# Kernel tuning notes

Hardware: AMD Instinct MI355X
Metric: run time of the kernel (lower is better)

The kernel has to match this reference:

```python
import jax, jax.numpy as jnp
import numpy as np

BS, NUM_VISIT, MAX_FEAT, MAX_TARGET = 32, 6, 12, 16
NUM_FEAT, NUM_REL, HIDDEN, REDUCED, OUT = 1992, 11, 128, 256, 90
GAMMA = 0.1


def setup_inputs() -> dict:
    key = jax.random.key(0)
    ks = jax.random.split(key, 20)
    u = lambda k, shape: jax.random.uniform(k, shape, dtype=jnp.float32)
    # one/multi-hot-like dense float inputs (per docstring)
    feat_index = (u(ks[0], (BS, NUM_VISIT, MAX_FEAT, NUM_FEAT)) < 0.01).astype(jnp.float32)
    neighbor_index = (u(ks[1], (BS, NUM_VISIT, MAX_FEAT, MAX_TARGET, NUM_FEAT)) < 0.001).astype(jnp.float32)
    rel_index = (u(ks[2], (BS, NUM_VISIT, MAX_FEAT, MAX_TARGET, NUM_REL)) < 0.2).astype(jnp.float32)
    # parameters (torch.rand init in the original; xavier for embedding)
    bound = float(np.sqrt(6.0 / (NUM_FEAT + HIDDEN)))
    emb_weight = jax.random.uniform(ks[3], (NUM_FEAT, HIDDEN), dtype=jnp.float32, minval=-bound, maxval=bound)
    return {
        "feat_index": feat_index,
        "neighbor_index": neighbor_index,
        "rel_index": rel_index,
        "emb_weight": emb_weight,
        "W_edge": u(ks[4], (NUM_REL, HIDDEN)),
        "W_v": u(ks[5], (REDUCED, HIDDEN)),
        "W_r": u(ks[6], (REDUCED, HIDDEN)),
        "b_v": u(ks[7], (REDUCED,)),
        "b_r": u(ks[8], (REDUCED,)),
        "W_alpha": u(ks[9], (NUM_FEAT,)),
        "b_alpha": u(ks[10], (MAX_FEAT,)),
        "W_beta": u(ks[11], (MAX_FEAT,)),
        "b_beta": u(ks[12], (NUM_VISIT,)),
        "W_l": u(ks[13], (REDUCED, REDUCED)),
        "b_l": u(ks[14], (REDUCED,)),
        "fc_W": u(ks[15], (OUT, 2 * REDUCED)) * 0.05,
        "fc_b": u(ks[16], (OUT,)) * 0.05,
    }


def reference(feat_index, neighbor_index, rel_index, emb_weight, W_edge, W_v, W_r,
              b_v, b_r, W_alpha, b_alpha, W_beta, b_beta, W_l, b_l, fc_W, fc_b):
    num_visit = feat_index.shape[1]
    # decay buffer lamb[i] = exp(-gamma*(num_visit - i))
    lamb = jnp.exp(-GAMMA * (num_visit - jnp.arange(num_visit, dtype=feat_index.dtype)))

    # node-level attention alpha: (b,v,m)
    alpha = jax.nn.softmax(jnp.einsum('n,bvmn->bvm', W_alpha, feat_index) + b_alpha)
    # visit-level attention beta: (b,v), modulated by temporal decay
    beta = jnp.tanh(jnp.einsum('m,bvm->bv', W_beta, alpha) + b_beta) * lamb

    # reduced node embeddings: (num_feat, reduced)
    reduced_emb = emb_weight @ W_v.T + b_v
    # attention-weighted neighbor aggregation; sum over targets t fused in
    attn = alpha * beta[:, :, None]                       # (b,v,m)
    node_agg = jnp.einsum('bvm,bvmtn,nr->bvmr', attn, neighbor_index, reduced_emb)

    # reduced edge (relation) embeddings: (num_rel, reduced)
    reduced_edge = W_edge @ W_r.T + b_r
    edge_agg = jnp.einsum('bvmtr,rd->bvmd', rel_index, reduced_edge)  # sum over t fused

    agg = node_agg + edge_agg                             # (b,v,m,reduced)
    # einsum('dd, bvfd -> bvfd') in torch takes the diagonal of W_l
    h = jax.nn.relu(jnp.diagonal(W_l) * agg + b_l)        # (b,v,m,reduced)

    h_g = h.sum(axis=(1, 2))                              # (b, reduced)
    # einsum('bvmn,bvmr->bvnr').sum(n).sum(v) == contract over v,m,n
    h_p = jnp.einsum('bvm,bvmr->br', feat_index.sum(-1), h)

    z_joint = jnp.concatenate([h_g, h_p], axis=-1)        # (b, 2*reduced)
    return jax.nn.sigmoid(z_joint @ fc_W.T + fc_b)
```

## Files before the change

### kernel.cpp

```cpp
#include <hip/hip_runtime.h>
#include <math.h>

#define BS   32
#define NV   6
#define MF   12
#define MT   16
#define NF   1992
#define NR   11
#define HID  128
#define RED  256
#define OUTD 90
#define GAMMA 0.1f
#define NZCAP 512

typedef float f4_t __attribute__((ext_vector_type(4)));

#define WS_HG    0
#define WS_HP    (WS_HG + BS*RED)
#define WS_ATTN  (WS_HP + BS*RED)
#define WS_FSUM  (WS_ATTN + BS*NV*MF)
#define WS_REMB  (WS_FSUM + BS*NV*MF)
#define WS_REDGE (WS_REMB + NF*RED)
#define WS_FCWT  (WS_REDGE + NR*RED)
#define WS_DIAG  (WS_FCWT + 2*RED*OUTD)

#define N_ZERO (2*BS*RED)
#define N_FCWT (2*RED*OUTD)
#define ZERO_BLOCKS (N_ZERO/256)
#define PREP2_BLOCKS ((N_FCWT+RED)/256)
#define ATTN_BLOCKS (BS*NV)
#define NPB 8
#define REMB_BLOCKS (NF/NPB)
#define REDGE_BLOCKS 2
#define K1_BLOCKS (ZERO_BLOCKS+PREP2_BLOCKS+ATTN_BLOCKS+REMB_BLOCKS+REDGE_BLOCKS)

__global__ __launch_bounds__(256) void k1_prep_attn_reduce(
        const float* __restrict__ feat, const float* __restrict__ W_alpha,
        const float* __restrict__ b_alpha, const float* __restrict__ W_beta,
        const float* __restrict__ b_beta,
        const float* __restrict__ emb, const float* __restrict__ W_edge,
        const float* __restrict__ W_v, const float* __restrict__ W_r,
        const float* __restrict__ b_v, const float* __restrict__ b_r,
        const float* __restrict__ fc_W, const float* __restrict__ W_l,
        float* __restrict__ ws_base, float* __restrict__ fcWT,
        float* __restrict__ diag,
        float* __restrict__ attn_ws, float* __restrict__ fsum_ws,
        float* __restrict__ remb, float* __restrict__ redge) {
    int blk = blockIdx.x;
    int tid = threadIdx.x;

    __shared__ float dot12[MF], fs12[MF];
    __shared__ float rows[NPB][HID];
    __shared__ float wT[32][RED + 1];

    if (blk < ZERO_BLOCKS) {
        ws_base[blk * 256 + tid] = 0.f;
        return;
    }
    blk -= ZERO_BLOCKS;

    if (blk < PREP2_BLOCKS) {
        int i = blk * 256 + tid;
        if (i < N_FCWT) {
            int jj = i / OUTD, o = i - jj * OUTD;
            fcWT[i] = fc_W[o * (2 * RED) + jj];
        } else {
            int j = i - N_FCWT;
            diag[j] = W_l[(size_t)j * RED + j];
        }
        return;
    }
    blk -= PREP2_BLOCKS;

    if (blk < ATTN_BLOCKS) {
        int bv   = blk;
        int v    = bv % NV;
        int wave = tid >> 6;
        int lane = tid & 63;
        const float* base = feat + (size_t)bv * MF * NF;
        for (int m = wave; m < MF; m += 4) {
            const float4* rw = (const float4*)(base + (size_t)m * NF);
            const float4* wa = (const float4*)W_alpha;
            float da = 0.f, fs = 0.f;
            for (int i = lane; i < NF / 4; i += 64) {
                float4 x = rw[i];
                float4 w = wa[i];
                da += w.x * x.x + w.y * x.y + w.z * x.z + w.w * x.w;
                fs += x.x + x.y + x.z + x.w;
            }
            #pragma unroll
            for (int off = 32; off > 0; off >>= 1) {
                da += __shfl_xor(da, off);
                fs += __shfl_xor(fs, off);
            }
            if (lane == 0) { dot12[m] = da; fs12[m] = fs; }
        }
        __syncthreads();
        if (tid == 0) {
            float logits[MF];
            float mx = -1e30f;
            for (int m = 0; m < MF; ++m) { logits[m] = dot12[m] + b_alpha[m]; mx = fmaxf(mx, logits[m]); }
            float s = 0.f;
            for (int m = 0; m < MF; ++m) { logits[m] = expf(logits[m] - mx); s += logits[m]; }
            float inv = 1.f / s;
            float bdot = 0.f;
            for (int m = 0; m < MF; ++m) { logits[m] *= inv; bdot += W_beta[m] * logits[m]; }
            float lamb = expf(-GAMMA * (float)(NV - v));
            float beta = tanhf(bdot + b_beta[v]) * lamb;
            for (int m = 0; m < MF; ++m) {
                attn_ws[bv * MF + m] = logits[m] * beta;
                fsum_ws[bv * MF + m] = fs12[m];
            }
        }
        return;
    }
    blk -= ATTN_BLOCKS;

    bool isEdge = (blk >= REMB_BLOCKS);
    const float* src  = isEdge ? W_edge : emb;
    const float* Wm   = isEdge ? W_r : W_v;
    const float* bias = isEdge ? b_r : b_v;
    float* dst        = isEdge ? redge : remb;
    int n0    = (isEdge ? (blk - REMB_BLOCKS) : blk) * NPB;
    int rowsN = isEdge ? min(NPB, NR - n0) : NPB;

    for (int idx = tid; idx < rowsN * HID; idx += 256)
        rows[idx >> 7][idx & 127] = src[(size_t)n0 * HID + idx];

    float bb = bias[tid];
    float a0 = bb, a1 = bb, a2 = bb, a3 = bb, a4 = bb, a5 = bb, a6 = bb, a7 = bb;
    for (int k0 = 0; k0 < HID; k0 += 32) {
        for (int idx = tid; idx < 32 * RED; idx += 256) {
            int rr = idx >> 5, kk = idx & 31;
            wT[kk][rr] = Wm[rr * HID + k0 + kk];
        }
        __syncthreads();
        #pragma unroll
        for (int kk = 0; kk < 32; ++kk) {
            float w = wT[kk][tid];
            int k = k0 + kk;
            a0 += rows[0][k] * w; a1 += rows[1][k] * w;
            a2 += rows[2][k] * w; a3 += rows[3][k] * w;
            a4 += rows[4][k] * w; a5 += rows[5][k] * w;
            a6 += rows[6][k] * w; a7 += rows[7][k] * w;
        }
        __syncthreads();
    }
    float* d0 = dst + (size_t)n0 * RED + tid;
    if (0 < rowsN) d0[0 * RED] = a0;
    if (1 < rowsN) d0[1 * RED] = a1;
    if (2 < rowsN) d0[2 * RED] = a2;
    if (3 < rowsN) d0[3 * RED] = a3;
    if (4 < rowsN) d0[4 * RED] = a4;
    if (5 < rowsN) d0[5 * RED] = a5;
    if (6 < rowsN) d0[6 * RED] = a6;
    if (7 < rowsN) d0[7 * RED] = a7;
}

__global__ __launch_bounds__(256) void k2_stream_gather(
        const float* __restrict__ nbr, const float* __restrict__ rel,
        const float* __restrict__ remb, const float* __restrict__ redge,
        const float* __restrict__ attn_ws, const float* __restrict__ fsum_ws,
        const float* __restrict__ diag, const float* __restrict__ b_l,
        float* __restrict__ h_g, float* __restrict__ h_p) {
    int bvm = blockIdx.x;
    int b   = bvm / (NV * MF);
    int tid = threadIdx.x;
    __shared__ int   nz_n[NZCAP];
    __shared__ float nz_v[NZCAP];
    __shared__ float rsum_s[NR];
    __shared__ int   cnt;
    __shared__ float s_attn, s_fsum;
    if (tid == 0) { cnt = 0; s_attn = attn_ws[bvm]; s_fsum = fsum_ws[bvm]; }

    int r = tid;
    float dg = diag[r];
    float bl = b_l[r];
    float rg[NR];
    #pragma unroll
    for (int j = 0; j < NR; ++j) rg[j] = redge[j * RED + r];

    const f4_t* base = (const f4_t*)(nbr + (size_t)bvm * MT * NF);
    f4_t a0 = (f4_t)(0.f);
    f4_t a1 = (f4_t)(0.f);
    const bool has1 = (tid + 256) < (NF / 4);
    #pragma unroll 4
    for (int t = 0; t < MT; ++t) {
        const f4_t* r4 = base + t * (NF / 4);
        a0 += __builtin_nontemporal_load(r4 + tid);
        if (has1) a1 += __builtin_nontemporal_load(r4 + tid + 256);
    }
    float rs = 0.f;
    if (tid < NR) {
        const float* rb = rel + (size_t)bvm * MT * NR;
        #pragma unroll
        for (int t = 0; t < MT; ++t) rs += rb[t * NR + tid];
    }
    __syncthreads();

    int nb = tid * 4;
    #pragma unroll
    for (int c4 = 0; c4 < 4; ++c4)
        if (a0[c4] != 0.f) {
            int p = atomicAdd(&cnt, 1);
            if (p < NZCAP) { nz_n[p] = nb + c4; nz_v[p] = a0[c4]; }
        }
    if (has1) {
        nb = (tid + 256) * 4;
        #pragma unroll
        for (int c4 = 0; c4 < 4; ++c4)
            if (a1[c4] != 0.f) {
                int p = atomicAdd(&cnt, 1);
                if (p < NZCAP) { nz_n[p] = nb + c4; nz_v[p] = a1[c4]; }
            }
    }
    if (tid < NR) rsum_s[tid] = rs;
    __syncthreads();

    int c = min(cnt, NZCAP);
    float g0 = 0.f, g1 = 0.f, g2 = 0.f, g3 = 0.f;
    int i = 0;
    for (; i + 4 <= c; i += 4) {
        g0 += nz_v[i]     * remb[(size_t)nz_n[i]     * RED + r];
        g1 += nz_v[i + 1] * remb[(size_t)nz_n[i + 1] * RED + r];
        g2 += nz_v[i + 2] * remb[(size_t)nz_n[i + 2] * RED + r];
        g3 += nz_v[i + 3] * remb[(size_t)nz_n[i + 3] * RED + r];
    }
    for (; i < c; ++i)
        g0 += nz_v[i] * remb[(size_t)nz_n[i] * RED + r];
    float node = (g0 + g1) + (g2 + g3);
    float edge = 0.f;
    #pragma unroll
    for (int j = 0; j < NR; ++j) edge += rsum_s[j] * rg[j];

    float agg = s_attn * node + edge;
    float h = fmaxf(0.f, dg * agg + bl);
    atomicAdd(&h_g[b * RED + r], h);
    atomicAdd(&h_p[b * RED + r], s_fsum * h);
}

__global__ __launch_bounds__(256) void k_out(
        const float* __restrict__ h_g, const float* __restrict__ h_p,
        const float* __restrict__ fcWT, const float* __restrict__ fc_b,
        float* __restrict__ out) {
    int b   = blockIdx.x;
    int tid = threadIdx.x;
    __shared__ float z[2 * RED];
    __shared__ float part[2][OUTD];
    for (int j = tid; j < RED; j += 256) {
        z[j]       = h_g[b * RED + j];
        z[RED + j] = h_p[b * RED + j];
    }
    __syncthreads();
    int o = tid & 127, half = tid >> 7;
    if (o < OUTD) {
        float acc = 0.f;
        int j0 = half * RED;
        #pragma unroll 8
        for (int j = j0; j < j0 + RED; ++j)
            acc += z[j] * fcWT[j * OUTD + o];
        part[half][o] = acc;
    }
    __syncthreads();
    if (tid < OUTD) {
        float acc = part[0][tid] + part[1][tid] + fc_b[tid];
        out[b * OUTD + tid] = 1.f / (1.f + expf(-acc));
    }
}

extern "C" void kernel_launch(void* const* d_in, const int* in_sizes, int n_in,
                              void* d_out, int out_size, void* d_ws, size_t ws_size,
                              hipStream_t stream) {
    const float* feat    = (const float*)d_in[0];
    const float* nbr     = (const float*)d_in[1];
    const float* rel     = (const float*)d_in[2];
    const float* emb     = (const float*)d_in[3];
    const float* W_edge  = (const float*)d_in[4];
    const float* W_v     = (const float*)d_in[5];
    const float* W_r     = (const float*)d_in[6];
    const float* b_v     = (const float*)d_in[7];
    const float* b_r     = (const float*)d_in[8];
    const float* W_alpha = (const float*)d_in[9];
    const float* b_alpha = (const float*)d_in[10];
    const float* W_beta  = (const float*)d_in[11];
    const float* b_beta  = (const float*)d_in[12];
    const float* W_l     = (const float*)d_in[13];
    const float* b_l     = (const float*)d_in[14];
    const float* fc_W    = (const float*)d_in[15];
    const float* fc_b    = (const float*)d_in[16];

    float* ws    = (float*)d_ws;
    float* hg    = ws + WS_HG;
    float* hp    = ws + WS_HP;
    float* attn  = ws + WS_ATTN;
    float* fsum  = ws + WS_FSUM;
    float* remb  = ws + WS_REMB;
    float* redge = ws + WS_REDGE;
    float* fcWT  = ws + WS_FCWT;
    float* diag  = ws + WS_DIAG;

    k1_prep_attn_reduce<<<K1_BLOCKS, 256, 0, stream>>>(
        feat, W_alpha, b_alpha, W_beta, b_beta,
        emb, W_edge, W_v, W_r, b_v, b_r, fc_W, W_l,
        ws, fcWT, diag, attn, fsum, remb, redge);
    k2_stream_gather<<<BS * NV * MF, 256, 0, stream>>>(
        nbr, rel, remb, redge, attn, fsum, diag, b_l, hg, hp);
    k_out<<<BS, 256, 0, stream>>>(hg, hp, fcWT, fc_b, (float*)d_out);
}
```

Baseline: 440.5 us.

## Fuse output layer into gather kernel via last-block counter; simplify embedding reduction

Removes the separate output kernel. Each gather block now bumps a per-batch completion counter, and the last block for a batch computes the final FC and sigmoid from the atomically accumulated h_g and h_p. This saves one launch and its tail. The reduced-embedding projection in k1 also drops the shared-memory transpose of W and its repeated syncs, with each thread reading its own W row as float4 from global memory. The cost is an extra atomic and fence per block, plus non-coalesced per-thread row reads of W.

```diff
diff --git a/kernel.cpp b/kernel.cpp
--- a/kernel.cpp
+++ b/kernel.cpp
@@ -23,11 +23,13 @@
 #define WS_REDGE (WS_REMB + NF*RED)
 #define WS_FCWT  (WS_REDGE + NR*RED)
 #define WS_DIAG  (WS_FCWT + 2*RED*OUTD)
+#define WS_DONE  (WS_DIAG + RED)
 
 #define N_ZERO (2*BS*RED)
+#define ZERO_ELEMS (N_ZERO + BS)
 #define N_FCWT (2*RED*OUTD)
-#define ZERO_BLOCKS (N_ZERO/256)
-#define PREP2_BLOCKS ((N_FCWT+RED)/256)
+#define ZERO_BLOCKS ((ZERO_ELEMS + 255)/256)
+#define PREP2_BLOCKS ((N_FCWT + RED)/256)
 #define ATTN_BLOCKS (BS*NV)
 #define NPB 8
 #define REMB_BLOCKS (NF/NPB)
@@ -42,19 +44,20 @@
         const float* __restrict__ W_v, const float* __restrict__ W_r,
         const float* __restrict__ b_v, const float* __restrict__ b_r,
         const float* __restrict__ fc_W, const float* __restrict__ W_l,
-        float* __restrict__ ws_base, float* __restrict__ fcWT,
-        float* __restrict__ diag,
+        float* __restrict__ ws_base, int* __restrict__ done_b,
+        float* __restrict__ fcWT, float* __restrict__ diag,
         float* __restrict__ attn_ws, float* __restrict__ fsum_ws,
         float* __restrict__ remb, float* __restrict__ redge) {
     int blk = blockIdx.x;
     int tid = threadIdx.x;
 
     __shared__ float dot12[MF], fs12[MF];
-    __shared__ float rows[NPB][HID];
-    __shared__ float wT[32][RED + 1];
+    __shared__ float4 rows4[NPB][HID / 4];
 
     if (blk < ZERO_BLOCKS) {
-        ws_base[blk * 256 + tid] = 0.f;
+        int i = blk * 256 + tid;
+        if (i < N_ZERO) ws_base[i] = 0.f;
+        else if (i < ZERO_ELEMS) done_b[i - N_ZERO] = 0;
         return;
     }
     blk -= ZERO_BLOCKS;
@@ -124,45 +127,42 @@
     int n0    = (isEdge ? (blk - REMB_BLOCKS) : blk) * NPB;
     int rowsN = isEdge ? min(NPB, NR - n0) : NPB;
 
-    for (int idx = tid; idx < rowsN * HID; idx += 256)
-        rows[idx >> 7][idx & 127] = src[(size_t)n0 * HID + idx];
-
-    float bb = bias[tid];
-    float a0 = bb, a1 = bb, a2 = bb, a3 = bb, a4 = bb, a5 = bb, a6 = bb, a7 = bb;
-    for (int k0 = 0; k0 < HID; k0 += 32) {
-        for (int idx = tid; idx < 32 * RED; idx += 256) {
-            int rr = idx >> 5, kk = idx & 31;
-            wT[kk][rr] = Wm[rr * HID + k0 + kk];
-        }
-        __syncthreads();
+    const float4* src4 = (const float4*)(src + (size_t)n0 * HID);
+    for (int idx = tid; idx < NPB * (HID / 4); idx += 256) {
+        int j = idx >> 5, k4 = idx & 31;
+        float4 z4 = {0.f, 0.f, 0.f, 0.f};
+        rows4[j][k4] = (j < rowsN) ? src4[idx] : z4;
+    }
+    __syncthreads();
+
+    int r = tid;
+    const float4* wv4 = (const float4*)(Wm + (size_t)r * HID);
+    float a[NPB];
+    float bb = bias[r];
+    #pragma unroll
+    for (int j = 0; j < NPB; ++j) a[j] = bb;
+    for (int k4 = 0; k4 < HID / 4; ++k4) {
+        float4 w = wv4[k4];
         #pragma unroll
-        for (int kk = 0; kk < 32; ++kk) {
-            float w = wT[kk][tid];
-            int k = k0 + kk;
-            a0 += rows[0][k] * w; a1 += rows[1][k] * w;
-            a2 += rows[2][k] * w; a3 += rows[3][k] * w;
-            a4 += rows[4][k] * w; a5 += rows[5][k] * w;
-            a6 += rows[6][k] * w; a7 += rows[7][k] * w;
-        }
-        __syncthreads();
-    }
-    float* d0 = dst + (size_t)n0 * RED + tid;
-    if (0 < rowsN) d0[0 * RED] = a0;
-    if (1 < rowsN) d0[1 * RED] = a1;
-    if (2 < rowsN) d0[2 * RED] = a2;
-    if (3 < rowsN) d0[3 * RED] = a3;
-    if (4 < rowsN) d0[4 * RED] = a4;
-    if (5 < rowsN) d0[5 * RED] = a5;
-    if (6 < rowsN) d0[6 * RED] = a6;
-    if (7 < rowsN) d0[7 * RED] = a7;
+        for (int j = 0; j < NPB; ++j) {
+            float4 e = rows4[j][k4];
+            a[j] += e.x * w.x + e.y * w.y + e.z * w.z + e.w * w.w;
+        }
+    }
+    float* d0 = dst + (size_t)n0 * RED + r;
+    #pragma unroll
+    for (int j = 0; j < NPB; ++j)
+        if (j < rowsN) d0[j * RED] = a[j];
 }
 
-__global__ __launch_bounds__(256) void k2_stream_gather(
+__global__ __launch_bounds__(256) void k2_stream_gather_out(
         const float* __restrict__ nbr, const float* __restrict__ rel,
         const float* __restrict__ remb, const float* __restrict__ redge,
         const float* __restrict__ attn_ws, const float* __restrict__ fsum_ws,
         const float* __restrict__ diag, const float* __restrict__ b_l,
-        float* __restrict__ h_g, float* __restrict__ h_p) {
+        const float* __restrict__ fcWT, const float* __restrict__ fc_b,
+        float* __restrict__ h_g, float* __restrict__ h_p,
+        int* __restrict__ done_b, float* __restrict__ out) {
     int bvm = blockIdx.x;
     int b   = bvm / (NV * MF);
     int tid = threadIdx.x;
@@ -170,8 +170,10 @@
     __shared__ float nz_v[NZCAP];
     __shared__ float rsum_s[NR];
     __shared__ int   cnt;
-    __shared__ float s_attn, s_fsum;
-    if (tid == 0) { cnt = 0; s_attn = attn_ws[bvm]; s_fsum = fsum_ws[bvm]; }
+    __shared__ int   lastflag;
+    __shared__ float z[2 * RED];
+    __shared__ float part[2][OUTD];
+    if (tid == 0) cnt = 0;
 
     int r = tid;
     float dg = diag[r];
@@ -233,23 +235,28 @@
     #pragma unroll
     for (int j = 0; j < NR; ++j) edge += rsum_s[j] * rg[j];
 
-    float agg = s_attn * node + edge;
+    float a  = attn_ws[bvm];
+    float fs = fsum_ws[bvm];
+    float agg = a * node + edge;
     float h = fmaxf(0.f, dg * agg + bl);
     atomicAdd(&h_g[b * RED + r], h);
-    atomicAdd(&h_p[b * RED + r], s_fsum * h);
-}
-
-__global__ __launch_bounds__(256) void k_out(
-        const float* __restrict__ h_g, const float* __restrict__ h_p,
-        const float* __restrict__ fcWT, const float* __restrict__ fc_b,
-        float* __restrict__ out) {
-    int b   = blockIdx.x;
-    int tid = threadIdx.x;
-    __shared__ float z[2 * RED];
-    __shared__ float part[2][OUTD];
+    atomicAdd(&h_p[b * RED + r], fs * h);
+
+    __syncthreads();
+    if (tid == 0) {
+        __threadfence();
+        int old = __hip_atomic_fetch_add(&done_b[b], 1,
+                                         __ATOMIC_ACQ_REL, __HIP_MEMORY_SCOPE_AGENT);
+        lastflag = (old == NV * MF - 1);
+    }
+    __syncthreads();
+    if (!lastflag) return;
+
     for (int j = tid; j < RED; j += 256) {
-        z[j]       = h_g[b * RED + j];
-        z[RED + j] = h_p[b * RED + j];
+        z[j]       = __hip_atomic_load(&h_g[b * RED + j], __ATOMIC_RELAXED,
+                                       __HIP_MEMORY_SCOPE_AGENT);
+        z[RED + j] = __hip_atomic_load(&h_p[b * RED + j], __ATOMIC_RELAXED,
+                                       __HIP_MEMORY_SCOPE_AGENT);
     }
     __syncthreads();
     int o = tid & 127, half = tid >> 7;
@@ -298,12 +305,13 @@
     float* redge = ws + WS_REDGE;
     float* fcWT  = ws + WS_FCWT;
     float* diag  = ws + WS_DIAG;
+    int*   done  = (int*)(ws + WS_DONE);
 
     k1_prep_attn_reduce<<<K1_BLOCKS, 256, 0, stream>>>(
         feat, W_alpha, b_alpha, W_beta, b_beta,
         emb, W_edge, W_v, W_r, b_v, b_r, fc_W, W_l,
-        ws, fcWT, diag, attn, fsum, remb, redge);
-    k2_stream_gather<<<BS * NV * MF, 256, 0, stream>>>(
-        nbr, rel, remb, redge, attn, fsum, diag, b_l, hg, hp);
-    k_out<<<BS, 256, 0, stream>>>(hg, hp, fcWT, fc_b, (float*)d_out);
+        ws, done, fcWT, diag, attn, fsum, remb, redge);
+    k2_stream_gather_out<<<BS * NV * MF, 256, 0, stream>>>(
+        nbr, rel, remb, redge, attn, fsum, diag, b_l, fcWT, fc_b,
+        hg, hp, done, (float*)d_out);
 }
```

New measurement: 616.1 us. 39.9% more time.
